# Performance work log

Hardware: AMD Instinct MI355X
Metric: run time of the kernel (lower is better)

The kernel has to match this reference:

```python
import jax, jax.numpy as jnp
import numpy as np

B, T, C, H = 4, 2048, 1024, 16
HD = C // H  # head dim = 64


def setup_inputs() -> dict:
    key = jax.random.key(0)
    k1, k2, k3, k4, k5 = jax.random.split(key, 5)
    s_in = 1.0 / np.sqrt(C)
    return {
        "x": jax.random.normal(k1, (B, T, C), dtype=jnp.float32),
        "W_attn": jax.random.uniform(k2, (C, 3 * C), dtype=jnp.float32, minval=-s_in, maxval=s_in),
        "b_attn": jax.random.uniform(k3, (3 * C,), dtype=jnp.float32, minval=-s_in, maxval=s_in),
        "W_proj": jax.random.uniform(k4, (C, C), dtype=jnp.float32, minval=-s_in, maxval=s_in),
        "b_proj": jax.random.uniform(k5, (C,), dtype=jnp.float32, minval=-s_in, maxval=s_in),
    }


def reference(x, W_attn, b_attn, W_proj, b_proj):
    Bx, Tx, Cx = x.shape
    qkv = x @ W_attn + b_attn                      # [B,T,3C]
    q, k, v = jnp.split(qkv, 3, axis=2)
    # [B,T,C] -> [B,H,T,HD]
    def heads(t):
        return t.reshape(Bx, Tx, H, HD).transpose(0, 2, 1, 3)
    q, k, v = heads(q), heads(k), heads(v)
    scale = 1.0 / np.sqrt(HD).astype(np.float32)
    att = jnp.einsum('bhqd,bhkd->bhqk', q, k) * scale
    causal = jnp.tril(jnp.ones((Tx, Tx), dtype=bool))
    att = jnp.where(causal[None, None], att, -jnp.inf)
    att = jax.nn.softmax(att, axis=-1)
    y = jnp.einsum('bhqk,bhkd->bhqd', att, v)      # [B,H,T,HD]
    y = y.transpose(0, 2, 1, 3).reshape(Bx, Tx, Cx)
    return y @ W_proj + b_proj
```

## Files before the change

### kernel.cpp

```cpp
#include <hip/hip_runtime.h>
#include <math.h>

#define Bn 4
#define Tn 2048
#define Cn 1024
#define Hn 16
#define HDn 64
#define Mn (Bn * Tn)

typedef unsigned short u16;
typedef unsigned int u32;
typedef __attribute__((ext_vector_type(8))) short bf16x8;
typedef __attribute__((ext_vector_type(8))) unsigned short us8;
typedef __attribute__((ext_vector_type(4))) float f32x4;

__device__ __forceinline__ float b2f(u16 u) {
    return __uint_as_float(((u32)u) << 16);
}
__device__ __forceinline__ u16 f2b(float f) {
    u32 u = __float_as_uint(f);
    return (u16)((u + 0x7FFFu + ((u >> 16) & 1u)) >> 16);
}

__device__ __forceinline__ int xcd_work(int bid, int nwg) {
    return (bid & 7) * (nwg >> 3) + (bid >> 3);
}

#define GLL(srcp, dstp)                                                     \
    __builtin_amdgcn_global_load_lds(                                       \
        (const __attribute__((address_space(1))) u32*)(srcp),               \
        (__attribute__((address_space(3))) u32*)(dstp), 16, 0, 0)

__global__ __launch_bounds__(256) void cvt_f32_bf16_kernel(
    const float4* __restrict__ in, ushort4* __restrict__ out, int n4)
{
    int i = blockIdx.x * 256 + threadIdx.x;
    if (i < n4) {
        float4 v = in[i];
        ushort4 o;
        o.x = f2b(v.x); o.y = f2b(v.y); o.z = f2b(v.z); o.w = f2b(v.w);
        out[i] = o;
    }
}

__global__ __launch_bounds__(256) void transpose_cvt_kernel(
    const float* __restrict__ in, u16* __restrict__ out, int R, int Cc)
{
    __shared__ u16 t[32][33];
    const int c0 = blockIdx.x * 32, r0 = blockIdx.y * 32;
    const int tx = threadIdx.x & 31, ty = threadIdx.x >> 5;
    #pragma unroll
    for (int i = 0; i < 32; i += 8)
        t[ty + i][tx] = f2b(in[(size_t)(r0 + ty + i) * Cc + c0 + tx]);
    __syncthreads();
    #pragma unroll
    for (int i = 0; i < 32; i += 8)
        out[(size_t)(c0 + ty + i) * R + r0 + tx] = t[tx][ty + i];
}

template <bool OUT_BF16, bool QKV_MODE>
__global__ __launch_bounds__(256) void gemm_bf16_kernel(
    const u16* __restrict__ A, const u16* __restrict__ BT,
    const float* __restrict__ bias,
    u16* __restrict__ outb, float* __restrict__ outf, u16* __restrict__ vTout,
    int N, int K, int nx)
{
    __shared__ u16 Al[128 * 32];
    __shared__ u16 Bl[128 * 32];

    const int tid = threadIdx.x;
    const int workid = xcd_work(blockIdx.x, gridDim.x);
    const int brow = (workid / nx) * 128;
    const int bcol = (workid % nx) * 128;
    const int w  = tid >> 6;
    const int wr = w >> 1, wc = w & 1;
    const int l  = tid & 63;
    const int lr = l & 15;
    const int lk = (l >> 4) << 3;

    f32x4 acc[4][4];
    #pragma unroll
    for (int m = 0; m < 4; ++m)
        #pragma unroll
        for (int n = 0; n < 4; ++n) acc[m][n] = (f32x4){0.f, 0.f, 0.f, 0.f};

    for (int k0 = 0; k0 < K; k0 += 32) {
        __syncthreads();
        #pragma unroll
        for (int i = 0; i < 2; ++i) {
            const int c   = i * 256 + tid;
            const int row = c >> 2;
            const int col = (c & 3) << 3;
            GLL(&A [(size_t)(brow + row) * K + k0 + col],
                &Al[(size_t)(i * 256 + (tid & 192)) * 8]);
            GLL(&BT[(size_t)(bcol + row) * K + k0 + col],
                &Bl[(size_t)(i * 256 + (tid & 192)) * 8]);
        }
        __syncthreads();

        bf16x8 a[4], b[4];
        #pragma unroll
        for (int m = 0; m < 4; ++m)
            a[m] = *(const bf16x8*)&Al[(wr * 64 + m * 16 + lr) * 32 + lk];
        #pragma unroll
        for (int n = 0; n < 4; ++n)
            b[n] = *(const bf16x8*)&Bl[(wc * 64 + n * 16 + lr) * 32 + lk];

        __builtin_amdgcn_s_setprio(1);
        #pragma unroll
        for (int m = 0; m < 4; ++m)
            #pragma unroll
            for (int n = 0; n < 4; ++n)
                acc[m][n] = __builtin_amdgcn_mfma_f32_16x16x32_bf16(
                    a[m], b[n], acc[m][n], 0, 0, 0);
        __builtin_amdgcn_s_setprio(0);
    }

    const int orow0 = brow + wr * 64 + ((l >> 4) << 2);
    const int ocol0 = bcol + wc * 64 + lr;
    if (QKV_MODE && bcol >= 2048) {
        #pragma unroll
        for (int n = 0; n < 4; ++n) {
            const int c = ocol0 + n * 16 - 2048;
            const float bv = bias[ocol0 + n * 16];
            #pragma unroll
            for (int m = 0; m < 4; ++m) {
                const int row0 = orow0 + m * 16;
                const int bb = row0 >> 11, t0 = row0 & 2047;
                ushort4 pk;
                pk.x = f2b(acc[m][n][0] + bv);
                pk.y = f2b(acc[m][n][1] + bv);
                pk.z = f2b(acc[m][n][2] + bv);
                pk.w = f2b(acc[m][n][3] + bv);
                *(ushort4*)&vTout[((size_t)bb * Cn + c) * Tn + t0] = pk;
            }
        }
    } else {
        #pragma unroll
        for (int n = 0; n < 4; ++n) {
            const int col = ocol0 + n * 16;
            const float bv = bias[col];
            #pragma unroll
            for (int m = 0; m < 4; ++m) {
                #pragma unroll
                for (int r = 0; r < 4; ++r) {
                    const int row = orow0 + m * 16 + r;
                    const float v = acc[m][n][r] + bv;
                    if (OUT_BF16) outb[(size_t)row * N + col] = f2b(v);
                    else          outf[(size_t)row * N + col] = v;
                }
            }
        }
    }
}

__device__ __forceinline__ void softmax_step(
    f32x4 S[4], float& m, float& ls, f32x4 O[4],
    u16* __restrict__ Prow, int g, int rsw, float S2)
{
    float ma = fmaxf(fmaxf(S[0][0], S[0][1]), fmaxf(S[0][2], S[0][3]));
    float mb = fmaxf(fmaxf(S[1][0], S[1][1]), fmaxf(S[1][2], S[1][3]));
    float mc = fmaxf(fmaxf(S[2][0], S[2][1]), fmaxf(S[2][2], S[2][3]));
    float md = fmaxf(fmaxf(S[3][0], S[3][1]), fmaxf(S[3][2], S[3][3]));
    float mt = fmaxf(fmaxf(ma, mb), fmaxf(mc, md));
    mt = fmaxf(mt, __shfl_xor(mt, 16));
    mt = fmaxf(mt, __shfl_xor(mt, 32));

    float lscale = 1.f;
    if (__any(!(mt <= m + 64.f))) {
        const float mn = fmaxf(m, mt);
        const float alpha = exp2f((m - mn) * S2);
        m = mn;
        float aO[4];
        #pragma unroll
        for (int r = 0; r < 4; ++r) aO[r] = __shfl(alpha, g * 4 + r);
        #pragma unroll
        for (int dc = 0; dc < 4; ++dc)
            #pragma unroll
            for (int r = 0; r < 4; ++r) O[dc][r] *= aO[r];
        lscale = alpha;
    }

    float lt = 0.f;
    #pragma unroll
    for (int kc = 0; kc < 4; ++kc) {
        const float p0 = exp2f((S[kc][0] - m) * S2);
        const float p1 = exp2f((S[kc][1] - m) * S2);
        const float p2 = exp2f((S[kc][2] - m) * S2);
        const float p3 = exp2f((S[kc][3] - m) * S2);
        lt += (p0 + p1) + (p2 + p3);
        u32 lo, hi;
        asm("v_cvt_pk_bf16_f32 %0, %1, %2" : "=v"(lo) : "v"(p0), "v"(p1));
        asm("v_cvt_pk_bf16_f32 %0, %1, %2" : "=v"(hi) : "v"(p2), "v"(p3));
        uint2 pk; pk.x = lo; pk.y = hi;
        *(uint2*)&Prow[((kc << 4) + (g << 2)) ^ rsw] = pk;
    }
    lt += __shfl_xor(lt, 16);
    lt += __shfl_xor(lt, 32);
    ls = ls * lscale + lt;
}

__global__ __launch_bounds__(256, 2) void attn_mfma5_kernel(
    const u16* __restrict__ qkvb, const u16* __restrict__ vT,
    u16* __restrict__ yb)
{
    __shared__ u16 Kb[2][64 * 64];
    __shared__ u16 Vb[2][64 * 64];
    __shared__ u16 Ps[4][32 * 64];

    const int tid = threadIdx.x;
    const int w   = tid >> 6;
    const int l   = tid & 63;
    const int l15 = l & 15;
    const int g   = l >> 4;
    const int work = xcd_work(blockIdx.x, 512);
    const int pr  = work & 7;
    const int bh  = work >> 3;
    const int b   = bh >> 4, h = bh & 15;

    const float S2 = 0.18033688f;

    const u16* Kg = qkvb + (size_t)(b * Tn) * (3 * Cn) + Cn + h * HDn;
    const u16* Vg = vT + (size_t)bh * HDn * Tn;

    const int srow = l >> 3;
    const int schk = ((l & 7) ^ srow) << 3;
    const int rloc = w * 16;
    const int rsw  = (l15 & 7) << 3;

    u16* const Prow0 = &Ps[w][(size_t)l15 << 6];
    u16* const Prow1 = Prow0 + (16 << 6);

    #pragma unroll 1
    for (int half = 0; half < 2; ++half) {
        const int qt = half ? (15 - pr) : pr;
        const int ktmax = 2 * qt + 2;
        const int qrow0 = qt * 128 + w * 32;

        const u16* Qp0 = qkvb + (size_t)(b * Tn + qrow0 + l15) * (3 * Cn)
                         + h * HDn + (g << 3);
        const u16* Qp1 = Qp0 + (size_t)16 * (3 * Cn);
        const bf16x8 qf00 = *(const bf16x8*)(Qp0);
        const bf16x8 qf01 = *(const bf16x8*)(Qp0 + 32);
        const bf16x8 qf10 = *(const bf16x8*)(Qp1);
        const bf16x8 qf11 = *(const bf16x8*)(Qp1 + 32);

        f32x4 O0[4], O1[4];
        float m0 = -INFINITY, m1 = -INFINITY, ls0 = 0.f, ls1 = 0.f;
        #pragma unroll
        for (int dc = 0; dc < 4; ++dc) {
            O0[dc] = (f32x4){0.f, 0.f, 0.f, 0.f};
            O1[dc] = (f32x4){0.f, 0.f, 0.f, 0.f};
        }

        #pragma unroll
        for (int jc = 0; jc < 2; ++jc) {
            const int rr = rloc + jc * 8;
            GLL(Kg + (size_t)(rr + srow) * (3 * Cn) + schk, &Kb[0][rr * 64]);
            GLL(Vg + (size_t)(rr + srow) * Tn + schk,       &Vb[0][rr * 64]);
        }
        __syncthreads();

        int cur = 0;
        for (int kt = 0; kt < ktmax; ++kt) {
            if (kt + 1 < ktmax) {
                #pragma unroll
                for (int jc = 0; jc < 2; ++jc) {
                    const int rr = rloc + jc * 8;
                    GLL(Kg + (size_t)((kt + 1) * 64 + rr + srow) * (3 * Cn) + schk,
                        &Kb[cur ^ 1][rr * 64]);
                    GLL(Vg + (size_t)(rr + srow) * Tn + (kt + 1) * 64 + schk,
                        &Vb[cur ^ 1][rr * 64]);
                }
            }
            const u16* Kc = Kb[cur];
            const u16* Vc = Vb[cur];

            if (kt * 64 <= qrow0 + 31) {
                f32x4 S0[4], S1[4];
                __builtin_amdgcn_s_setprio(1);
                #pragma unroll
                for (int kc = 0; kc < 4; ++kc) {
                    const bf16x8 k0 =
                        *(const bf16x8*)&Kc[(kc * 16 + l15) * 64 + ((g << 3) ^ rsw)];
                    const bf16x8 k1 =
                        *(const bf16x8*)&Kc[(kc * 16 + l15) * 64 + ((32 + (g << 3)) ^ rsw)];
                    f32x4 z0 = (f32x4){0.f, 0.f, 0.f, 0.f};
                    z0 = __builtin_amdgcn_mfma_f32_16x16x32_bf16(k0, qf00, z0, 0, 0, 0);
                    S0[kc] = __builtin_amdgcn_mfma_f32_16x16x32_bf16(k1, qf01, z0, 0, 0, 0);
                    f32x4 z1 = (f32x4){0.f, 0.f, 0.f, 0.f};
                    z1 = __builtin_amdgcn_mfma_f32_16x16x32_bf16(k0, qf10, z1, 0, 0, 0);
                    S1[kc] = __builtin_amdgcn_mfma_f32_16x16x32_bf16(k1, qf11, z1, 0, 0, 0);
                }
                __builtin_amdgcn_s_setprio(0);

                if (kt * 64 + 63 > qrow0) {
                    const int qg = qrow0 + l15;
                    #pragma unroll
                    for (int kc = 0; kc < 4; ++kc)
                        #pragma unroll
                        for (int r = 0; r < 4; ++r)
                            if (kt * 64 + kc * 16 + g * 4 + r > qg)
                                S0[kc][r] = -INFINITY;
                }
                if (kt * 64 + 63 > qrow0 + 16) {
                    const int qg = qrow0 + 16 + l15;
                    #pragma unroll
                    for (int kc = 0; kc < 4; ++kc)
                        #pragma unroll
                        for (int r = 0; r < 4; ++r)
                            if (kt * 64 + kc * 16 + g * 4 + r > qg)
                                S1[kc][r] = -INFINITY;
                }

                softmax_step(S0, m0, ls0, O0, Prow0, g, rsw, S2);
                softmax_step(S1, m1, ls1, O1, Prow1, g, rsw, S2);

                __builtin_amdgcn_s_setprio(1);
                #pragma unroll
                for (int hf = 0; hf < 2; ++hf) {
                    const bf16x8 pf0 =
                        *(const bf16x8*)&Prow0[((hf << 5) + (g << 3)) ^ rsw];
                    const bf16x8 pf1 =
                        *(const bf16x8*)&Prow1[((hf << 5) + (g << 3)) ^ rsw];
                    #pragma unroll
                    for (int dc = 0; dc < 4; ++dc) {
                        const bf16x8 vf = *(const bf16x8*)
                            &Vc[(dc * 16 + l15) * 64 + ((((hf << 2) + g) << 3) ^ rsw)];
                        O0[dc] = __builtin_amdgcn_mfma_f32_16x16x32_bf16(pf0, vf, O0[dc], 0, 0, 0);
                        O1[dc] = __builtin_amdgcn_mfma_f32_16x16x32_bf16(pf1, vf, O1[dc], 0, 0, 0);
                    }
                }
                __builtin_amdgcn_s_setprio(0);
            }

            __syncthreads();
            cur ^= 1;
        }

        #pragma unroll
        for (int r = 0; r < 4; ++r) {
            const float inv0 = __builtin_amdgcn_rcpf(__shfl(ls0, g * 4 + r));
            const size_t ro0 =
                (size_t)(b * Tn + qrow0 + g * 4 + r) * Cn + h * HDn;
            #pragma unroll
            for (int dc = 0; dc < 4; ++dc)
                yb[ro0 + dc * 16 + l15] = f2b(O0[dc][r] * inv0);
            const float inv1 = __builtin_amdgcn_rcpf(__shfl(ls1, g * 4 + r));
            const size_t ro1 =
                (size_t)(b * Tn + qrow0 + 16 + g * 4 + r) * Cn + h * HDn;
            #pragma unroll
            for (int dc = 0; dc < 4; ++dc)
                yb[ro1 + dc * 16 + l15] = f2b(O1[dc][r] * inv1);
        }
    }
}

extern "C" void kernel_launch(void* const* d_in, const int* in_sizes, int n_in,
                              void* d_out, int out_size, void* d_ws, size_t ws_size,
                              hipStream_t stream)
{
    const float* x      = (const float*)d_in[0];
    const float* W_attn = (const float*)d_in[1];
    const float* b_attn = (const float*)d_in[2];
    const float* W_proj = (const float*)d_in[3];
    const float* b_proj = (const float*)d_in[4];
    float* out = (float*)d_out;

    u16* xb   = (u16*)d_ws;
    u16* WaT  = xb   + (size_t)Mn * Cn;
    u16* WpT  = WaT  + (size_t)3 * Cn * Cn;
    u16* qkvb = WpT  + (size_t)Cn * Cn;
    u16* yb   = qkvb + (size_t)Mn * 3 * Cn;
    u16* vT   = yb   + (size_t)Mn * Cn;

    cvt_f32_bf16_kernel<<<(Mn * Cn / 4 + 255) / 256, 256, 0, stream>>>(
        (const float4*)x, (ushort4*)xb, Mn * Cn / 4);

    transpose_cvt_kernel<<<dim3(3 * Cn / 32, Cn / 32), 256, 0, stream>>>(
        W_attn, WaT, Cn, 3 * Cn);
    transpose_cvt_kernel<<<dim3(Cn / 32, Cn / 32), 256, 0, stream>>>(
        W_proj, WpT, Cn, Cn);

    gemm_bf16_kernel<true, true><<<24 * 64, 256, 0, stream>>>(
        xb, WaT, b_attn, qkvb, nullptr, vT, 3 * Cn, Cn, 24);

    attn_mfma5_kernel<<<512, 256, 0, stream>>>(qkvb, vT, yb);

    gemm_bf16_kernel<false, false><<<8 * 64, 256, 0, stream>>>(
        yb, WpT, b_proj, nullptr, out, nullptr, Cn, Cn, 8);
}
```

Measured before the change: 214.7 us.

## Switch attention to 32x32x16 MFMA and keep P in registers via permlane swaps

The attention kernel moves from 16x16x32 to 32x32x16 bf16 MFMA tiles computing S transposed (keys x queries), so each lane owns one query column and the softmax max/sum needs only a single cross-half shuffle. The probability tile is no longer staged through LDS: packed bf16 values are rearranged in registers with v_permlane32_swap into the A-operand layout for the PV MFMA, which removes the Ps shared buffer and its LDS writes and reads. This adds permlane instructions and larger accumulator register footprints, which could affect register pressure under the 2-waves launch bound.

```diff
diff --git a/kernel.cpp b/kernel.cpp
--- a/kernel.cpp
+++ b/kernel.cpp
@@ -13,6 +13,8 @@
 typedef __attribute__((ext_vector_type(8))) short bf16x8;
 typedef __attribute__((ext_vector_type(8))) unsigned short us8;
 typedef __attribute__((ext_vector_type(4))) float f32x4;
+typedef __attribute__((ext_vector_type(16))) float f32x16;
+typedef __attribute__((ext_vector_type(4))) unsigned int u32x4;
 
 __device__ __forceinline__ float b2f(u16 u) {
     return __uint_as_float(((u32)u) << 16);
@@ -20,6 +22,14 @@
 __device__ __forceinline__ u16 f2b(float f) {
     u32 u = __float_as_uint(f);
     return (u16)((u + 0x7FFFu + ((u >> 16) & 1u)) >> 16);
+}
+__device__ __forceinline__ u32 cvtpk(float a, float b) {
+    u32 d;
+    asm("v_cvt_pk_bf16_f32 %0, %1, %2" : "=v"(d) : "v"(a), "v"(b));
+    return d;
+}
+__device__ __forceinline__ void pswap(u32& a, u32& b) {
+    asm("v_permlane32_swap_b32 %0, %1" : "+v"(a), "+v"(b));
 }
 
 __device__ __forceinline__ int xcd_work(int bid, int nwg) {
@@ -154,65 +164,18 @@
     }
 }
 
-__device__ __forceinline__ void softmax_step(
-    f32x4 S[4], float& m, float& ls, f32x4 O[4],
-    u16* __restrict__ Prow, int g, int rsw, float S2)
-{
-    float ma = fmaxf(fmaxf(S[0][0], S[0][1]), fmaxf(S[0][2], S[0][3]));
-    float mb = fmaxf(fmaxf(S[1][0], S[1][1]), fmaxf(S[1][2], S[1][3]));
-    float mc = fmaxf(fmaxf(S[2][0], S[2][1]), fmaxf(S[2][2], S[2][3]));
-    float md = fmaxf(fmaxf(S[3][0], S[3][1]), fmaxf(S[3][2], S[3][3]));
-    float mt = fmaxf(fmaxf(ma, mb), fmaxf(mc, md));
-    mt = fmaxf(mt, __shfl_xor(mt, 16));
-    mt = fmaxf(mt, __shfl_xor(mt, 32));
-
-    float lscale = 1.f;
-    if (__any(!(mt <= m + 64.f))) {
-        const float mn = fmaxf(m, mt);
-        const float alpha = exp2f((m - mn) * S2);
-        m = mn;
-        float aO[4];
-        #pragma unroll
-        for (int r = 0; r < 4; ++r) aO[r] = __shfl(alpha, g * 4 + r);
-        #pragma unroll
-        for (int dc = 0; dc < 4; ++dc)
-            #pragma unroll
-            for (int r = 0; r < 4; ++r) O[dc][r] *= aO[r];
-        lscale = alpha;
-    }
-
-    float lt = 0.f;
-    #pragma unroll
-    for (int kc = 0; kc < 4; ++kc) {
-        const float p0 = exp2f((S[kc][0] - m) * S2);
-        const float p1 = exp2f((S[kc][1] - m) * S2);
-        const float p2 = exp2f((S[kc][2] - m) * S2);
-        const float p3 = exp2f((S[kc][3] - m) * S2);
-        lt += (p0 + p1) + (p2 + p3);
-        u32 lo, hi;
-        asm("v_cvt_pk_bf16_f32 %0, %1, %2" : "=v"(lo) : "v"(p0), "v"(p1));
-        asm("v_cvt_pk_bf16_f32 %0, %1, %2" : "=v"(hi) : "v"(p2), "v"(p3));
-        uint2 pk; pk.x = lo; pk.y = hi;
-        *(uint2*)&Prow[((kc << 4) + (g << 2)) ^ rsw] = pk;
-    }
-    lt += __shfl_xor(lt, 16);
-    lt += __shfl_xor(lt, 32);
-    ls = ls * lscale + lt;
-}
-
-__global__ __launch_bounds__(256, 2) void attn_mfma5_kernel(
+__global__ __launch_bounds__(256, 2) void attn_mfma6_kernel(
     const u16* __restrict__ qkvb, const u16* __restrict__ vT,
     u16* __restrict__ yb)
 {
     __shared__ u16 Kb[2][64 * 64];
     __shared__ u16 Vb[2][64 * 64];
-    __shared__ u16 Ps[4][32 * 64];
 
     const int tid = threadIdx.x;
     const int w   = tid >> 6;
     const int l   = tid & 63;
-    const int l15 = l & 15;
-    const int g   = l >> 4;
+    const int q31 = l & 31;
+    const int hi  = l >> 5;
     const int work = xcd_work(blockIdx.x, 512);
     const int pr  = work & 7;
     const int bh  = work >> 3;
@@ -226,32 +189,25 @@
     const int srow = l >> 3;
     const int schk = ((l & 7) ^ srow) << 3;
     const int rloc = w * 16;
-    const int rsw  = (l15 & 7) << 3;
-
-    u16* const Prow0 = &Ps[w][(size_t)l15 << 6];
-    u16* const Prow1 = Prow0 + (16 << 6);
+    const int rsw8 = q31 & 7;
 
     #pragma unroll 1
     for (int half = 0; half < 2; ++half) {
         const int qt = half ? (15 - pr) : pr;
         const int ktmax = 2 * qt + 2;
         const int qrow0 = qt * 128 + w * 32;
-
-        const u16* Qp0 = qkvb + (size_t)(b * Tn + qrow0 + l15) * (3 * Cn)
-                         + h * HDn + (g << 3);
-        const u16* Qp1 = Qp0 + (size_t)16 * (3 * Cn);
-        const bf16x8 qf00 = *(const bf16x8*)(Qp0);
-        const bf16x8 qf01 = *(const bf16x8*)(Qp0 + 32);
-        const bf16x8 qf10 = *(const bf16x8*)(Qp1);
-        const bf16x8 qf11 = *(const bf16x8*)(Qp1 + 32);
-
-        f32x4 O0[4], O1[4];
-        float m0 = -INFINITY, m1 = -INFINITY, ls0 = 0.f, ls1 = 0.f;
-        #pragma unroll
-        for (int dc = 0; dc < 4; ++dc) {
-            O0[dc] = (f32x4){0.f, 0.f, 0.f, 0.f};
-            O1[dc] = (f32x4){0.f, 0.f, 0.f, 0.f};
-        }
+        const int qglob = qrow0 + q31;
+
+        const u16* Qp = qkvb + (size_t)(b * Tn + qglob) * (3 * Cn)
+                        + h * HDn + hi * 8;
+        bf16x8 qf[4];
+        #pragma unroll
+        for (int c = 0; c < 4; ++c) qf[c] = *(const bf16x8*)(Qp + c * 16);
+
+        f32x16 O0, O1;
+        #pragma unroll
+        for (int r = 0; r < 16; ++r) { O0[r] = 0.f; O1[r] = 0.f; }
+        float m = -INFINITY, ls = 0.f;
 
         #pragma unroll
         for (int jc = 0; jc < 2; ++jc) {
@@ -277,58 +233,83 @@
             const u16* Vc = Vb[cur];
 
             if (kt * 64 <= qrow0 + 31) {
-                f32x4 S0[4], S1[4];
+                f32x16 S0, S1;
+                #pragma unroll
+                for (int r = 0; r < 16; ++r) { S0[r] = 0.f; S1[r] = 0.f; }
                 __builtin_amdgcn_s_setprio(1);
                 #pragma unroll
-                for (int kc = 0; kc < 4; ++kc) {
-                    const bf16x8 k0 =
-                        *(const bf16x8*)&Kc[(kc * 16 + l15) * 64 + ((g << 3) ^ rsw)];
-                    const bf16x8 k1 =
-                        *(const bf16x8*)&Kc[(kc * 16 + l15) * 64 + ((32 + (g << 3)) ^ rsw)];
-                    f32x4 z0 = (f32x4){0.f, 0.f, 0.f, 0.f};
-                    z0 = __builtin_amdgcn_mfma_f32_16x16x32_bf16(k0, qf00, z0, 0, 0, 0);
-                    S0[kc] = __builtin_amdgcn_mfma_f32_16x16x32_bf16(k1, qf01, z0, 0, 0, 0);
-                    f32x4 z1 = (f32x4){0.f, 0.f, 0.f, 0.f};
-                    z1 = __builtin_amdgcn_mfma_f32_16x16x32_bf16(k0, qf10, z1, 0, 0, 0);
-                    S1[kc] = __builtin_amdgcn_mfma_f32_16x16x32_bf16(k1, qf11, z1, 0, 0, 0);
+                for (int c = 0; c < 4; ++c) {
+                    const int co = ((2 * c + hi) ^ rsw8) << 3;
+                    const bf16x8 k0 = *(const bf16x8*)&Kc[q31 * 64 + co];
+                    const bf16x8 k1 = *(const bf16x8*)&Kc[(32 + q31) * 64 + co];
+                    S0 = __builtin_amdgcn_mfma_f32_32x32x16_bf16(k0, qf[c], S0, 0, 0, 0);
+                    S1 = __builtin_amdgcn_mfma_f32_32x32x16_bf16(k1, qf[c], S1, 0, 0, 0);
                 }
                 __builtin_amdgcn_s_setprio(0);
 
                 if (kt * 64 + 63 > qrow0) {
-                    const int qg = qrow0 + l15;
                     #pragma unroll
-                    for (int kc = 0; kc < 4; ++kc)
-                        #pragma unroll
-                        for (int r = 0; r < 4; ++r)
-                            if (kt * 64 + kc * 16 + g * 4 + r > qg)
-                                S0[kc][r] = -INFINITY;
-                }
-                if (kt * 64 + 63 > qrow0 + 16) {
-                    const int qg = qrow0 + 16 + l15;
+                    for (int r = 0; r < 16; ++r) {
+                        const int kl = kt * 64 + (r & 3) + 8 * (r >> 2) + 4 * hi;
+                        if (kl > qglob)      S0[r] = -INFINITY;
+                        if (kl + 32 > qglob) S1[r] = -INFINITY;
+                    }
+                }
+
+                float mt = S0[0];
+                #pragma unroll
+                for (int r = 1; r < 16; ++r) mt = fmaxf(mt, S0[r]);
+                #pragma unroll
+                for (int r = 0; r < 16; ++r) mt = fmaxf(mt, S1[r]);
+                mt = fmaxf(mt, __shfl_xor(mt, 32));
+
+                float lscale = 1.f;
+                if (__any(mt > m + 64.f)) {
+                    const float mn = fmaxf(m, mt);
+                    const float alpha = exp2f((m - mn) * S2);
+                    m = mn; lscale = alpha;
                     #pragma unroll
-                    for (int kc = 0; kc < 4; ++kc)
-                        #pragma unroll
-                        for (int r = 0; r < 4; ++r)
-                            if (kt * 64 + kc * 16 + g * 4 + r > qg)
-                                S1[kc][r] = -INFINITY;
-                }
-
-                softmax_step(S0, m0, ls0, O0, Prow0, g, rsw, S2);
-                softmax_step(S1, m1, ls1, O1, Prow1, g, rsw, S2);
+                    for (int r = 0; r < 16; ++r) {
+                        const int qloc = (r & 3) + 8 * (r >> 2) + 4 * hi;
+                        const float ar = __shfl(alpha, qloc);
+                        O0[r] *= ar; O1[r] *= ar;
+                    }
+                }
+
+                float lt = 0.f;
+                u32 w0[8], w1[8];
+                #pragma unroll
+                for (int i = 0; i < 8; ++i) {
+                    const float p0 = exp2f((S0[2 * i]     - m) * S2);
+                    const float p1 = exp2f((S0[2 * i + 1] - m) * S2);
+                    const float p2 = exp2f((S1[2 * i]     - m) * S2);
+                    const float p3 = exp2f((S1[2 * i + 1] - m) * S2);
+                    lt += (p0 + p1) + (p2 + p3);
+                    w0[i] = cvtpk(p0, p1);
+                    w1[i] = cvtpk(p2, p3);
+                }
+                lt += __shfl_xor(lt, 32);
+                ls = ls * lscale + lt;
 
                 __builtin_amdgcn_s_setprio(1);
                 #pragma unroll
-                for (int hf = 0; hf < 2; ++hf) {
-                    const bf16x8 pf0 =
-                        *(const bf16x8*)&Prow0[((hf << 5) + (g << 3)) ^ rsw];
-                    const bf16x8 pf1 =
-                        *(const bf16x8*)&Prow1[((hf << 5) + (g << 3)) ^ rsw];
+                for (int t2 = 0; t2 < 2; ++t2) {
                     #pragma unroll
-                    for (int dc = 0; dc < 4; ++dc) {
-                        const bf16x8 vf = *(const bf16x8*)
-                            &Vc[(dc * 16 + l15) * 64 + ((((hf << 2) + g) << 3) ^ rsw)];
-                        O0[dc] = __builtin_amdgcn_mfma_f32_16x16x32_bf16(pf0, vf, O0[dc], 0, 0, 0);
-                        O1[dc] = __builtin_amdgcn_mfma_f32_16x16x32_bf16(pf1, vf, O1[dc], 0, 0, 0);
+                    for (int c1 = 0; c1 < 2; ++c1) {
+                        u32 a0 = t2 ? w1[4 * c1 + 0] : w0[4 * c1 + 0];
+                        u32 b0 = t2 ? w1[4 * c1 + 2] : w0[4 * c1 + 2];
+                        u32 a1 = t2 ? w1[4 * c1 + 1] : w0[4 * c1 + 1];
+                        u32 b1 = t2 ? w1[4 * c1 + 3] : w0[4 * c1 + 3];
+                        pswap(a0, b0);
+                        pswap(a1, b1);
+                        u32x4 fr; fr.x = a0; fr.y = a1; fr.z = b0; fr.w = b1;
+                        const bf16x8 pf = __builtin_bit_cast(bf16x8, fr);
+                        const int c = t2 * 2 + c1;
+                        const int co = ((2 * c + hi) ^ rsw8) << 3;
+                        const bf16x8 v0 = *(const bf16x8*)&Vc[q31 * 64 + co];
+                        const bf16x8 v1 = *(const bf16x8*)&Vc[(32 + q31) * 64 + co];
+                        O0 = __builtin_amdgcn_mfma_f32_32x32x16_bf16(pf, v0, O0, 0, 0, 0);
+                        O1 = __builtin_amdgcn_mfma_f32_32x32x16_bf16(pf, v1, O1, 0, 0, 0);
                     }
                 }
                 __builtin_amdgcn_s_setprio(0);
@@ -339,19 +320,12 @@
         }
 
         #pragma unroll
-        for (int r = 0; r < 4; ++r) {
-            const float inv0 = __builtin_amdgcn_rcpf(__shfl(ls0, g * 4 + r));
-            const size_t ro0 =
-                (size_t)(b * Tn + qrow0 + g * 4 + r) * Cn + h * HDn;
-            #pragma unroll
-            for (int dc = 0; dc < 4; ++dc)
-                yb[ro0 + dc * 16 + l15] = f2b(O0[dc][r] * inv0);
-            const float inv1 = __builtin_amdgcn_rcpf(__shfl(ls1, g * 4 + r));
-            const size_t ro1 =
-                (size_t)(b * Tn + qrow0 + 16 + g * 4 + r) * Cn + h * HDn;
-            #pragma unroll
-            for (int dc = 0; dc < 4; ++dc)
-                yb[ro1 + dc * 16 + l15] = f2b(O1[dc][r] * inv1);
+        for (int r = 0; r < 16; ++r) {
+            const int qloc = (r & 3) + 8 * (r >> 2) + 4 * hi;
+            const float inv = __builtin_amdgcn_rcpf(__shfl(ls, qloc));
+            u16* yp = yb + (size_t)(b * Tn + qrow0 + qloc) * Cn + h * HDn + q31;
+            yp[0]  = f2b(O0[r] * inv);
+            yp[32] = f2b(O1[r] * inv);
         }
     }
 }
@@ -385,7 +359,7 @@
     gemm_bf16_kernel<true, true><<<24 * 64, 256, 0, stream>>>(
         xb, WaT, b_attn, qkvb, nullptr, vT, 3 * Cn, Cn, 24);
 
-    attn_mfma5_kernel<<<512, 256, 0, stream>>>(qkvb, vT, yb);
+    attn_mfma6_kernel<<<512, 256, 0, stream>>>(qkvb, vT, yb);
 
     gemm_bf16_kernel<false, false><<<8 * 64, 256, 0, stream>>>(
         yb, WpT, b_proj, nullptr, out, nullptr, Cn, Cn, 8);
```

Result: faster. 202.4 us (-5.7%).
